# Kernel optimization log

Hardware: AMD Instinct MI355X
Metric: run time of the kernel (lower is better)

The kernel has to match this reference:

```python
import jax, jax.numpy as jnp
import numpy as np

H = 32  # hidden size

def _lstm_layer(x, Wih, Whh, bih, bhh):
    # x: [B, T, in]; Wih: [4H, in]; Whh: [4H, H]; biases: [4H]
    # Precompute input contribution for all timesteps (one big GEMM).
    xg = jnp.einsum('bti,gi->btg', x, Wih) + (bih + bhh)  # [B, T, 4H]
    B = x.shape[0]
    h0 = jnp.zeros((B, H), x.dtype)
    c0 = jnp.zeros((B, H), x.dtype)

    def step(carry, xt):
        h, c = carry
        g = xt + h @ Whh.T                      # [B, 4H]
        i, f, gg, o = jnp.split(g, 4, axis=-1)   # PyTorch gate order: i,f,g,o
        i = jax.nn.sigmoid(i)
        f = jax.nn.sigmoid(f)
        gg = jnp.tanh(gg)
        o = jax.nn.sigmoid(o)
        c = f * c + i * gg
        h = o * jnp.tanh(c)
        return (h, c), h

    (_, _), hs = jax.lax.scan(step, (h0, c0), jnp.swapaxes(xg, 0, 1))  # hs: [T, B, H]
    return jnp.swapaxes(hs, 0, 1)  # [B, T, H]


def setup_inputs() -> dict:
    key = jax.random.key(0)
    ks = jax.random.split(key, 11)
    B, T = 4096, 1024
    s = 1.0 / np.sqrt(H)  # PyTorch LSTM init scale
    f32 = jnp.float32
    return {
        'x':    jax.random.normal(ks[0], (B, T, 1), dtype=f32),
        'Wih0': jax.random.uniform(ks[1], (4 * H, 1), dtype=f32, minval=-s, maxval=s),
        'Whh0': jax.random.uniform(ks[2], (4 * H, H), dtype=f32, minval=-s, maxval=s),
        'bih0': jax.random.uniform(ks[3], (4 * H,), dtype=f32, minval=-s, maxval=s),
        'bhh0': jax.random.uniform(ks[4], (4 * H,), dtype=f32, minval=-s, maxval=s),
        'Wih1': jax.random.uniform(ks[5], (4 * H, H), dtype=f32, minval=-s, maxval=s),
        'Whh1': jax.random.uniform(ks[6], (4 * H, H), dtype=f32, minval=-s, maxval=s),
        'bih1': jax.random.uniform(ks[7], (4 * H,), dtype=f32, minval=-s, maxval=s),
        'bhh1': jax.random.uniform(ks[8], (4 * H,), dtype=f32, minval=-s, maxval=s),
        'Wfc':  jax.random.uniform(ks[9], (1, H), dtype=f32, minval=-s, maxval=s),
        'bfc':  jax.random.uniform(ks[10], (1,), dtype=f32, minval=-s, maxval=s),
    }


def reference(x, Wih0, Whh0, bih0, bhh0, Wih1, Whh1, bih1, bhh1, Wfc, bfc):
    h1 = _lstm_layer(x, Wih0, Whh0, bih0, bhh0)   # [B, T, H]
    h2 = _lstm_layer(h1, Wih1, Whh1, bih1, bhh1)  # [B, T, H]
    last = h2[:, -1, :]                            # [B, H]
    return last @ Wfc.T + bfc                      # [B, 1]
```

## Files before the change

### kernel.cpp

```cpp
#include <hip/hip_runtime.h>

#define HSZ  32
#define TLEN 1024
#define PS   40

typedef _Float16 half8 __attribute__((ext_vector_type(8)));
typedef float    f32x4 __attribute__((ext_vector_type(4)));

__device__ __forceinline__ float rcp_f(float x){ return __builtin_amdgcn_rcpf(x); }
__device__ __forceinline__ float exp2_f(float x){ return __builtin_amdgcn_exp2f(x); }
#define SCL_S (-1.442695040888963f)
#define SCL_T ( 2.885390081777927f)

__device__ __forceinline__ f32x4 mfma16(half8 a, half8 b, f32x4 c){
  return __builtin_amdgcn_mfma_f32_16x16x32_f16(a, b, c, 0, 0, 0);
}
__device__ __forceinline__ void lds_barrier(){
  asm volatile("s_waitcnt lgkmcnt(0)\n\ts_barrier" ::: "memory");
}

#define ACT4(A0,A1,A2,A3, CV, OV)                              \
  float OV;                                                    \
  { float Zi_ = exp2_f(A0), Zf_ = exp2_f(A1);                  \
    float Zg_ = exp2_f(A2), Zo_ = exp2_f(A3);                  \
    float di_ = 1.f+Zi_, df_ = 1.f+Zf_;                        \
    float dg_ = 1.f+Zg_, dq_ = 1.f+Zo_;                        \
    float r1_ = rcp_f(di_*df_);                                \
    float IV_ = r1_*df_, FV_ = r1_*di_;                        \
    float r2_ = rcp_f(dg_*dq_);                                \
    float GV_ = fmaf(-2.f, r2_*dq_, 1.f); OV = r2_*dg_;        \
    CV = fmaf(FV_, CV, IV_*GV_); }

#define HOUT(CV, OV, HV)                                       \
  { float Zc_ = exp2_f(SCL_T*(CV));                            \
    float rc_ = rcp_f(1.f + Zc_);                              \
    HV = fmaf(-2.f, rc_*(OV), OV); }

__global__ __launch_bounds__(512, 2) void lstm2_sp(
    const float* __restrict__ x,
    const float* __restrict__ Wih0, const float* __restrict__ Whh0,
    const float* __restrict__ bih0, const float* __restrict__ bhh0,
    const float* __restrict__ Wih1, const float* __restrict__ Whh1,
    const float* __restrict__ bih1, const float* __restrict__ bhh1,
    const float* __restrict__ Wfc,  const float* __restrict__ bfc,
    float* __restrict__ out, int Tn)
{
  __shared__ __align__(16) _Float16 H0[16*PS];
  __shared__ __align__(16) _Float16 H1[16*PS];
  __shared__ float sc[32*17];

  const int tid = threadIdx.x;
  const int w   = tid >> 6;
  const int l   = tid & 63;
  const int c   = l & 15;
  const int g   = l >> 4;
  const int s   = 4*w + g;
  const int b0  = blockIdx.x * 16;

  const int prow = 32*(c & 3) + 4*w + (c >> 2);
  const float sA = ((c & 3) == 2) ? SCL_T : SCL_S;
  half8 W0h, W0l, WIh, WIl, WHh, WHl;
  {
    const float* p0 = Whh0 + prow*HSZ + 8*g;
    const float* p1 = Wih1 + prow*HSZ + 8*g;
    const float* p2 = Whh1 + prow*HSZ + 8*g;
    #pragma unroll
    for (int j = 0; j < 8; ++j){
      float v0 = p0[j]*sA, v1 = p1[j]*sA, v2 = p2[j]*sA;
      _Float16 a = (_Float16)v0; W0h[j] = a; W0l[j] = (_Float16)(v0 - (float)a);
      _Float16 b = (_Float16)v1; WIh[j] = b; WIl[j] = (_Float16)(v1 - (float)b);
      _Float16 d = (_Float16)v2; WHh[j] = d; WHl[j] = (_Float16)(v2 - (float)d);
    }
  }
  const float scj[4] = {SCL_S, SCL_S, SCL_T, SCL_S};
  float wx[4], bs0[4];
  f32x4 bias1;
  #pragma unroll
  for (int j = 0; j < 4; ++j){
    int r    = 32*j + s;
    wx[j]    = Wih0[r] * scj[j];
    bs0[j]   = (bih0[r] + bhh0[r]) * scj[j];
    bias1[j] = (bih1[r] + bhh1[r]) * scj[j];
  }
  const f32x4 zero4 = {0.f, 0.f, 0.f, 0.f};

  const int wrI = c*PS + s;
  const int rdI = c*PS + 8*g;

  const float* xp = x + (size_t)(b0 + c) * Tn;
  float c0 = 0.f, c1 = 0.f;

  {
    float x0 = xp[0];
    float a0 = fmaf(x0, wx[0], bs0[0]);
    float a1 = fmaf(x0, wx[1], bs0[1]);
    float a2 = fmaf(x0, wx[2], bs0[2]);
    float a3 = fmaf(x0, wx[3], bs0[3]);
    ACT4(a0, a1, a2, a3, c0, o0_);
    float h0;
    HOUT(c0, o0_, h0);
    H0[wrI] = (_Float16)h0;
  }
  __syncthreads();
  half8 Bh0 = *(const half8*)&H0[rdI];
  half8 Bh1 = {};
  float xv = xp[1];

  float h1v = 0.f;
  const int Tm1 = Tn - 1;

  for (int t = 0; t < Tm1; ++t){
    int xi = t + 2; xi = (xi > Tm1) ? Tm1 : xi;
    float xn = xp[xi];

    f32x4 u, vv;
    u  = mfma16(WHh, Bh1, bias1);
    u  = mfma16(WHl, Bh1, u);
    vv = mfma16(WIh, Bh0, zero4);
    vv = mfma16(WIl, Bh0, vv);
    f32x4 a = u + vv;
    ACT4(a[0], a[1], a[2], a[3], c1, o1_);
    HOUT(c1, o1_, h1v);
    H1[wrI] = (_Float16)h1v;

    lds_barrier();

    f32x4 e;
    e[0] = fmaf(xv, wx[0], bs0[0]);
    e[1] = fmaf(xv, wx[1], bs0[1]);
    e[2] = fmaf(xv, wx[2], bs0[2]);
    e[3] = fmaf(xv, wx[3], bs0[3]);
    e = mfma16(W0h, Bh0, e);
    e = mfma16(W0l, Bh0, e);
    Bh1 = *(const half8*)&H1[rdI];
    ACT4(e[0], e[1], e[2], e[3], c0, o0_);
    float h0;
    HOUT(c0, o0_, h0);
    H0[wrI] = (_Float16)h0;

    lds_barrier();

    Bh0 = *(const half8*)&H0[rdI];
    xv = xn;
  }

  {
    f32x4 u, vv;
    u  = mfma16(WHh, Bh1, bias1);
    u  = mfma16(WHl, Bh1, u);
    vv = mfma16(WIh, Bh0, zero4);
    vv = mfma16(WIl, Bh0, vv);
    f32x4 a = u + vv;
    ACT4(a[0], a[1], a[2], a[3], c1, o1_);
    HOUT(c1, o1_, h1v);
  }

  sc[s*17 + c] = h1v;
  __syncthreads();
  if (tid < 16){
    float acc = bfc[0];
    #pragma unroll 8
    for (int k = 0; k < HSZ; ++k) acc = fmaf(sc[k*17 + tid], Wfc[k], acc);
    out[b0 + tid] = acc;
  }
}

extern "C" void kernel_launch(void* const* d_in, const int* in_sizes, int n_in,
                              void* d_out, int out_size, void* d_ws, size_t ws_size,
                              hipStream_t stream) {
  const float* x    = (const float*)d_in[0];
  const float* Wih0 = (const float*)d_in[1];
  const float* Whh0 = (const float*)d_in[2];
  const float* bih0 = (const float*)d_in[3];
  const float* bhh0 = (const float*)d_in[4];
  const float* Wih1 = (const float*)d_in[5];
  const float* Whh1 = (const float*)d_in[6];
  const float* bih1 = (const float*)d_in[7];
  const float* bhh1 = (const float*)d_in[8];
  const float* Wfc  = (const float*)d_in[9];
  const float* bfc  = (const float*)d_in[10];
  float* out = (float*)d_out;

  const int Tn = TLEN;
  const int B  = in_sizes[0] / Tn;

  dim3 block(512);
  dim3 grid(B / 16);
  hipLaunchKernelGGL(lstm2_sp, grid, block, 0, stream,
                     x, Wih0, Whh0, bih0, bhh0, Wih1, Whh1, bih1, bhh1,
                     Wfc, bfc, out, Tn);
}
```

Baseline: 499.3 us.

## Skew the two LSTM layers into one step with double-buffered hidden state

Restructures the time loop so layer 1 at step t-1 and layer 0 at step t are computed in the same iteration. Their MFMAs and activations become independent, and the LDS hidden-state buffers are double-buffered so each step needs one barrier instead of two. The final tanh calls are paired so two of them share one reciprocal. The kernel also carries two identical copies (P and Q) of the recurrence over the same batch columns and keeps one per half of the columns, which doubles the per-step math and LDS traffic in exchange for more independent instructions.

```diff
diff --git a/kernel.cpp b/kernel.cpp
--- a/kernel.cpp
+++ b/kernel.cpp
@@ -20,7 +20,6 @@
 }
 
 #define ACT4(A0,A1,A2,A3, CV, OV)                              \
-  float OV;                                                    \
   { float Zi_ = exp2_f(A0), Zf_ = exp2_f(A1);                  \
     float Zg_ = exp2_f(A2), Zo_ = exp2_f(A3);                  \
     float di_ = 1.f+Zi_, df_ = 1.f+Zf_;                        \
@@ -31,12 +30,14 @@
     float GV_ = fmaf(-2.f, r2_*dq_, 1.f); OV = r2_*dg_;        \
     CV = fmaf(FV_, CV, IV_*GV_); }
 
-#define HOUT(CV, OV, HV)                                       \
-  { float Zc_ = exp2_f(SCL_T*(CV));                            \
-    float rc_ = rcp_f(1.f + Zc_);                              \
-    HV = fmaf(-2.f, rc_*(OV), OV); }
-
-__global__ __launch_bounds__(512, 2) void lstm2_sp(
+#define TANHPAIR(CA, CB, OA, OB, HA, HB)                       \
+  { float ZA_ = exp2_f(SCL_T*(CA)), ZB_ = exp2_f(SCL_T*(CB));  \
+    float dA_ = 1.f+ZA_, dB_ = 1.f+ZB_;                        \
+    float re_ = rcp_f(dA_*dB_);                                \
+    float qA_ = re_*dB_*(OA), qB_ = re_*dA_*(OB);              \
+    HA = fmaf(-2.f, qA_, OA); HB = fmaf(-2.f, qB_, OB); }
+
+__global__ __launch_bounds__(512, 2) void lstm2_dual(
     const float* __restrict__ x,
     const float* __restrict__ Wih0, const float* __restrict__ Whh0,
     const float* __restrict__ bih0, const float* __restrict__ bhh0,
@@ -45,9 +46,8 @@
     const float* __restrict__ Wfc,  const float* __restrict__ bfc,
     float* __restrict__ out, int Tn)
 {
-  __shared__ __align__(16) _Float16 H0[16*PS];
-  __shared__ __align__(16) _Float16 H1[16*PS];
-  __shared__ float sc[32*17];
+  __shared__ __align__(16) _Float16 hP[2][2][16*PS];
+  __shared__ __align__(16) _Float16 hQ[2][2][16*PS];
 
   const int tid = threadIdx.x;
   const int w   = tid >> 6;
@@ -87,8 +87,14 @@
   const int wrI = c*PS + s;
   const int rdI = c*PS + 8*g;
 
+  for (int i = tid; i < 2*2*16*PS; i += 512){
+    (&hP[0][0][0])[i] = (_Float16)0.0f;
+    (&hQ[0][0][0])[i] = (_Float16)0.0f;
+  }
+
   const float* xp = x + (size_t)(b0 + c) * Tn;
-  float c0 = 0.f, c1 = 0.f;
+  float c0P = 0.f, c1P = 0.f, c0Q = 0.f, c1Q = 0.f;
+  float h1P = 0.f, h1Q = 0.f;
 
   {
     float x0 = xp[0];
@@ -96,66 +102,82 @@
     float a1 = fmaf(x0, wx[1], bs0[1]);
     float a2 = fmaf(x0, wx[2], bs0[2]);
     float a3 = fmaf(x0, wx[3], bs0[3]);
+    float c0 = 0.f, o0_;
     ACT4(a0, a1, a2, a3, c0, o0_);
-    float h0;
-    HOUT(c0, o0_, h0);
-    H0[wrI] = (_Float16)h0;
+    float Zc = exp2_f(SCL_T * c0);
+    float rc = rcp_f(1.f + Zc);
+    float h0 = fmaf(-2.f, rc * o0_, o0_);
+    __syncthreads();
+    hP[0][0][wrI] = (_Float16)h0;
+    hQ[0][0][wrI] = (_Float16)h0;
+    c0P = c0; c0Q = c0;
   }
   __syncthreads();
-  half8 Bh0 = *(const half8*)&H0[rdI];
-  half8 Bh1 = {};
+  half8 BP0 = *(const half8*)&hP[0][0][rdI];
+  half8 BP1 = *(const half8*)&hP[0][1][rdI];
+  half8 BQ0 = *(const half8*)&hQ[0][0][rdI];
+  half8 BQ1 = *(const half8*)&hQ[0][1][rdI];
   float xv = xp[1];
 
-  float h1v = 0.f;
-  const int Tm1 = Tn - 1;
-
-  for (int t = 0; t < Tm1; ++t){
-    int xi = t + 2; xi = (xi > Tm1) ? Tm1 : xi;
-    float xn = xp[xi];
-
-    f32x4 u, vv;
-    u  = mfma16(WHh, Bh1, bias1);
-    u  = mfma16(WHl, Bh1, u);
-    vv = mfma16(WIh, Bh0, zero4);
-    vv = mfma16(WIl, Bh0, vv);
-    f32x4 a = u + vv;
-    ACT4(a[0], a[1], a[2], a[3], c1, o1_);
-    HOUT(c1, o1_, h1v);
-    H1[wrI] = (_Float16)h1v;
-
-    lds_barrier();
-
-    f32x4 e;
-    e[0] = fmaf(xv, wx[0], bs0[0]);
-    e[1] = fmaf(xv, wx[1], bs0[1]);
-    e[2] = fmaf(xv, wx[2], bs0[2]);
-    e[3] = fmaf(xv, wx[3], bs0[3]);
-    e = mfma16(W0h, Bh0, e);
-    e = mfma16(W0l, Bh0, e);
-    Bh1 = *(const half8*)&H1[rdI];
-    ACT4(e[0], e[1], e[2], e[3], c0, o0_);
-    float h0;
-    HOUT(c0, o0_, h0);
-    H0[wrI] = (_Float16)h0;
-
-    lds_barrier();
-
-    Bh0 = *(const half8*)&H0[rdI];
-    xv = xn;
-  }
-
-  {
-    f32x4 u, vv;
-    u  = mfma16(WHh, Bh1, bias1);
-    u  = mfma16(WHl, Bh1, u);
-    vv = mfma16(WIh, Bh0, zero4);
-    vv = mfma16(WIl, Bh0, vv);
-    f32x4 a = u + vv;
-    ACT4(a[0], a[1], a[2], a[3], c1, o1_);
-    HOUT(c1, o1_, h1v);
-  }
-
-  sc[s*17 + c] = h1v;
+#define STEP(PQ, TIDX)                                                     \
+  {                                                                        \
+    float xn = xp[(TIDX)];               \
+                                  \
+    f32x4 eQ;                                                              \
+    eQ[0] = fmaf(xv, wx[0], bs0[0]);                                       \
+    eQ[1] = fmaf(xv, wx[1], bs0[1]);                                       \
+    eQ[2] = fmaf(xv, wx[2], bs0[2]);                                       \
+    eQ[3] = fmaf(xv, wx[3], bs0[3]);                                       \
+    f32x4 uQ = mfma16(WHh, BQ1, bias1);                                    \
+    f32x4 vQ = mfma16(WIh, BQ0, zero4);                                    \
+    eQ = mfma16(W0h, BQ0, eQ);                                             \
+    uQ = mfma16(WHl, BQ1, uQ);                                             \
+    vQ = mfma16(WIl, BQ0, vQ);                                             \
+    eQ = mfma16(W0l, BQ0, eQ);                                             \
+    f32x4 aQ = uQ + vQ;                                                    \
+    float o1Q_, o0Q_, h0Qv;                                                \
+    ACT4(aQ[0],aQ[1],aQ[2],aQ[3], c1Q, o1Q_);                              \
+    ACT4(eQ[0],eQ[1],eQ[2],eQ[3], c0Q, o0Q_);                              \
+    TANHPAIR(c1Q, c0Q, o1Q_, o0Q_, h1Q, h0Qv);                             \
+    hQ[(PQ)][1][wrI] = (_Float16)h1Q;                                      \
+    hQ[(PQ)][0][wrI] = (_Float16)h0Qv;                                     \
+                                   \
+    f32x4 eP;                                                              \
+    eP[0] = fmaf(xv, wx[0], bs0[0]);                                       \
+    eP[1] = fmaf(xv, wx[1], bs0[1]);                                       \
+    eP[2] = fmaf(xv, wx[2], bs0[2]);                                       \
+    eP[3] = fmaf(xv, wx[3], bs0[3]);                                       \
+    f32x4 uP = mfma16(WHh, BP1, bias1);                                    \
+    f32x4 vP = mfma16(WIh, BP0, zero4);                                    \
+    eP = mfma16(W0h, BP0, eP);                                             \
+    uP = mfma16(WHl, BP1, uP);                                             \
+    vP = mfma16(WIl, BP0, vP);                                             \
+    eP = mfma16(W0l, BP0, eP);                                             \
+    f32x4 aP = uP + vP;                                                    \
+    float o1P_, o0P_, h0Pv;                                                \
+    ACT4(aP[0],aP[1],aP[2],aP[3], c1P, o1P_);                              \
+    ACT4(eP[0],eP[1],eP[2],eP[3], c0P, o0P_);                              \
+    TANHPAIR(c1P, c0P, o1P_, o0P_, h1P, h0Pv);                             \
+    hP[(PQ)][1][wrI] = (_Float16)h1P;                                      \
+    hP[(PQ)][0][wrI] = (_Float16)h0Pv;                                     \
+    lds_barrier();                                                         \
+                  \
+    BQ0 = *(const half8*)&hQ[(PQ)][0][rdI];                                \
+    BQ1 = *(const half8*)&hQ[(PQ)][1][rdI];                                \
+    BP0 = *(const half8*)&hP[(PQ)][0][rdI];                                \
+    BP1 = *(const half8*)&hP[(PQ)][1][rdI];                                \
+    xv = xn;                                                               \
+  }
+
+  for (int T0 = 0; T0 < Tn; T0 += 2){
+    STEP(1, (T0+2 < Tn) ? T0+2 : Tn-1);
+    STEP(0, (T0+3 < Tn) ? T0+3 : Tn-1);
+  }
+#undef STEP
+
+  __syncthreads();
+  float* sc = (float*)&hP[0][0][0];
+  sc[s*17 + c] = (c < 8) ? h1P : h1Q;
   __syncthreads();
   if (tid < 16){
     float acc = bfc[0];
@@ -186,7 +208,7 @@
 
   dim3 block(512);
   dim3 grid(B / 16);
-  hipLaunchKernelGGL(lstm2_sp, grid, block, 0, stream,
+  hipLaunchKernelGGL(lstm2_dual, grid, block, 0, stream,
                      x, Wih0, Whh0, bih0, bhh0, Wih1, Whh1, bih1, bhh1,
                      Wfc, bfc, out, Tn);
 }
```

After: 731.4 us. +46.5%, slower.
